# Optimization experiments

Measured on AMD Instinct MI355X. Metric: run time of the kernel, lower is better.

The kernel has to match this reference:

```python
import jax, jax.numpy as jnp
import numpy as np

K = 3
UP_H, UP_W = 120, 160  # up_size
RES_H, RES_W = UP_H + K - 1, UP_W + K - 1  # bilinear target before valid depthwise conv


def _bilinear_align_corners(x, out_h, out_w):
    """PyTorch UpsamplingBilinear2d (align_corners=True). x: [B,C,H,W]."""
    B, C, H, W = x.shape
    # row interpolation
    hy = jnp.arange(out_h, dtype=x.dtype) * ((H - 1) / (out_h - 1))
    y0 = jnp.floor(hy).astype(jnp.int32)
    y1 = jnp.minimum(y0 + 1, H - 1)
    fy = (hy - y0.astype(x.dtype))[None, None, :, None]
    x = x[:, :, y0, :] * (1 - fy) + x[:, :, y1, :] * fy  # [B,C,out_h,W]
    # col interpolation
    wx = jnp.arange(out_w, dtype=x.dtype) * ((W - 1) / (out_w - 1))
    x0i = jnp.floor(wx).astype(jnp.int32)
    x1i = jnp.minimum(x0i + 1, W - 1)
    fx = (wx - x0i.astype(x.dtype))[None, None, None, :]
    return x[:, :, :, x0i] * (1 - fx) + x[:, :, :, x1i] * fx  # [B,C,out_h,out_w]


def setup_inputs() -> dict:
    key = jax.random.key(0)
    k1, k2, k3 = jax.random.split(key, 3)
    C_in, C_out = 256, 128
    x = jax.random.normal(k1, (8, C_in, 60, 80), dtype=jnp.float32)
    # depthwise kernel [C_in, 1, K, K], pointwise [C_out, C_in]; fan-in-ish scale
    w_dw = jax.random.normal(k2, (C_in, 1, K, K), dtype=jnp.float32) * (1.0 / K)
    w_pw = jax.random.normal(k3, (C_out, C_in), dtype=jnp.float32) * (1.0 / np.sqrt(C_in))
    return {"x": x, "w_dw": w_dw, "w_pw": w_pw}


def reference(x, w_dw, w_pw):
    C_in = x.shape[1]
    # 1) bilinear upsample (align_corners=True) to (UP_H+K-1, UP_W+K-1)
    up = _bilinear_align_corners(x, RES_H, RES_W)
    # 2) depthwise KxK conv, stride 1, VALID padding -> [B,C_in,UP_H,UP_W]
    dw = jax.lax.conv_general_dilated(
        up, w_dw, window_strides=(1, 1), padding="VALID",
        dimension_numbers=("NCHW", "OIHW", "NCHW"),
        feature_group_count=C_in)
    # 3) pointwise 1x1 conv -> [B,C_out,UP_H,UP_W]
    return jnp.einsum("bchw,oc->bohw", dw, w_pw)
```

## Files before the change

kernel.cpp:

```cpp
#include <hip/hip_runtime.h>

#define CIN  256
#define HIN  60
#define WIN  80
#define UPH  120
#define UPW  160
#define COUT 128
#define NPIX (UPH*UPW)

typedef __bf16 bf16x8 __attribute__((ext_vector_type(8)));
typedef float  floatx4 __attribute__((ext_vector_type(4)));

__global__ void wpw_cvt(const float* __restrict__ wpw, __bf16* __restrict__ wpwb)
{
    int i = (blockIdx.x * blockDim.x + threadIdx.x) * 8;
    float4 a = *(const float4*)(wpw + i);
    float4 b = *(const float4*)(wpw + i + 4);
    bf16x8 o = {(__bf16)a.x,(__bf16)a.y,(__bf16)a.z,(__bf16)a.w,
                (__bf16)b.x,(__bf16)b.y,(__bf16)b.z,(__bf16)b.w};
    *(bf16x8*)(wpwb + i) = o;
}

#define F_NT  512
#define KC    32
#define NCK   (CIN/KC)
#define QPC   45
#define NIT   (KC*QPC)
#define NITP  1472

__global__ __launch_bounds__(F_NT, 4) void fused_kernel(
    const float* __restrict__ x,
    const float* __restrict__ wdw,
    const __bf16* __restrict__ wpwb,
    float* __restrict__ out)
{
    __shared__ __align__(16) float  s_xf[2][NITP*4];
    __shared__ __align__(16) __bf16 s_dw[2][160*KC];
    __shared__ float s_A[KC*19];
    __shared__ float s_rw[18];

    const int tid = threadIdx.x;

    const int bid = blockIdx.x;
    const int wg  = (bid & 7) * 120 + (bid >> 3);
    const int wt  = wg & 1;
    const int t2  = wg >> 1;
    const int ht  = t2 % 60;
    const int b   = t2 / 60;

    const int h0 = ht * 2, w0 = wt * 80;
    const float HS = 59.0f / 121.0f, WS = 79.0f / 161.0f;
    const int rbase = (int)((float)h0 * HS);
    const int c0a = ((int)((float)w0 * WS)) & ~3;

    if (tid < 18) {
        int ahh = tid / 9, t = tid - ahh * 9;
        int i3 = t / 3, dy = t - i3 * 3;
        int ybh = (int)((float)(h0 + ahh) * HS);
        float hy = (float)(h0 + ahh + i3) * HS;
        int y0 = (int)hy; float fy = hy - (float)y0;
        int y1 = min(y0 + 1, HIN - 1);
        s_rw[tid] = ((y0 - ybh) == dy ? 1.f - fy : 0.f)
                  + ((y1 - ybh) == dy ? fy : 0.f);
    }

    const int lane = tid & 63, wave = tid >> 6;
    const int quad = lane >> 4, l16 = lane & 15;

    const int ch  = tid & 31;
    const int seg = (tid >> 5) & 7;
    const int hh  = tid >> 8;
    const int rbh = (int)((float)(h0 + hh) * HS) - rbase;

    const int ciA = tid / 18, tA = tid - ciA * 18;
    const int hhA = tA / 9, dA = tA - hhA * 9, dyA = dA / 3, jA = dA - dyA * 3;
    const bool hasB = (tid < 64);
    const int iB = tid + 512, ciB = iB / 18, tB = iB - ciB * 18;
    const int hhB = tB / 9, dB = tB - hhB * 9, dyB = dB / 3, jB = dB - dyB * 3;

    const float* xb = x + (size_t)b * CIN * (HIN * WIN);

    auto dma = [&](int cb, int buf) {
        #pragma unroll
        for (int k = 0; k < 3; k++) {
            int ws = (k * 8 + wave) * 64;
            if (ws < NIT) {
                int it = ws + lane;
                it = it < NIT ? it : NIT - 1;
                int c  = it / QPC;
                int t  = it - c * QPC;
                t = t < 44 ? t : 43;
                int r = t / 11, q = t - r * 11;
                int gy = min(rbase + r, HIN - 1);
                const float* src = xb + (size_t)(cb + c) * (HIN * WIN)
                                 + gy * WIN + c0a + q * 4;
                __builtin_amdgcn_global_load_lds(
                    (const __attribute__((address_space(1))) void*)src,
                    (__attribute__((address_space(3))) void*)(&s_xf[buf][ws * 4]),
                    16, 0, 0);
            }
        }
    };

    float wA0, wA1, wA2, wB0 = 0.f, wB1 = 0.f, wB2 = 0.f;
    auto loadw = [&](int cb) {
        const float* wp = wdw + (size_t)(cb + ciA) * 9 + jA;
        wA0 = wp[0]; wA1 = wp[3]; wA2 = wp[6];
        if (hasB) {
            const float* wq = wdw + (size_t)(cb + ciB) * 9 + jB;
            wB0 = wq[0]; wB1 = wq[3]; wB2 = wq[6];
        }
    };

    floatx4 acc[10];
    #pragma unroll
    for (int n = 0; n < 10; n++) acc[n] = (floatx4){0.f, 0.f, 0.f, 0.f};

    dma(0, 0);
    loadw(0);
    __syncthreads();

    for (int p = 0; p < NCK; p++) {
        s_A[ciA * 19 + tA] = s_rw[hhA*9 + dyA]     * wA0
                           + s_rw[hhA*9 + 3 + dyA] * wA1
                           + s_rw[hhA*9 + 6 + dyA] * wA2;
        if (hasB)
            s_A[ciB * 19 + tB] = s_rw[hhB*9 + dyB]     * wB0
                               + s_rw[hhB*9 + 3 + dyB] * wB1
                               + s_rw[hhB*9 + 6 + dyB] * wB2;

        asm volatile("s_waitcnt vmcnt(0)" ::: "memory");
        __syncthreads();

        if (p < NCK - 1) {
            dma((p + 1) * KC, (p + 1) & 1);
            loadw((p + 1) * KC);
        }

        float Ar[3][3];
        #pragma unroll
        for (int dy = 0; dy < 3; dy++)
            #pragma unroll
            for (int j = 0; j < 3; j++)
                Ar[dy][j] = s_A[ch * 19 + hh * 9 + dy * 3 + j];

        const float* xfp = s_xf[p & 1];
        const int chb = ch * 180;
        __bf16* dwp = s_dw[p & 1];

        #pragma unroll
        for (int g = 0; g < 2; g++) {
            const int ub = w0 + seg * 10 + g * 5;
            float fx[7]; int ci[7];
            #pragma unroll
            for (int j = 0; j < 7; j++) {
                float wx = (float)(ub + j) * WS;
                int x0 = (int)wx;
                fx[j] = wx - (float)x0;
                ci[j] = chb + (x0 - c0a);
            }
            float d[5] = {0.f, 0.f, 0.f, 0.f, 0.f};
            #pragma unroll
            for (int dy = 0; dy < 3; dy++) {
                const float* rp = xfp + (rbh + dy) * 44;
                float cx[7];
                #pragma unroll
                for (int j = 0; j < 7; j++) {
                    float lo = rp[ci[j]], hi = rp[ci[j] + 1];
                    cx[j] = fmaf(fx[j], hi - lo, lo);
                }
                float A0 = Ar[dy][0], A1 = Ar[dy][1], A2 = Ar[dy][2];
                #pragma unroll
                for (int i = 0; i < 5; i++)
                    d[i] = fmaf(A0, cx[i],
                           fmaf(A1, cx[i+1],
                           fmaf(A2, cx[i+2], d[i])));
            }
            #pragma unroll
            for (int i = 0; i < 5; i++) {
                int px = hh * 80 + seg * 10 + g * 5 + i;
                dwp[px * KC + (ch ^ ((px & 3) << 3))] = (__bf16)d[i];
            }
        }

        bf16x8 af = *(const bf16x8*)(wpwb + (size_t)(wave * 16 + l16) * CIN
                                     + p * KC + quad * 8);

        __syncthreads();

        const char* dwb = (const char*)dwp;
        const int dwrd_base = l16 * 64 + ((quad * 16) ^ ((l16 & 3) << 4));
        #pragma unroll
        for (int n = 0; n < 10; n++) {
            bf16x8 bf = *(const bf16x8*)(dwb + dwrd_base + n * 1024);
            acc[n] = __builtin_amdgcn_mfma_f32_16x16x32_bf16(af, bf, acc[n], 0, 0, 0);
        }
    }

    float* ob = out + (size_t)(b * COUT + wave * 16 + quad * 4) * NPIX
              + (size_t)h0 * UPW + w0;
    #pragma unroll
    for (int n = 0; n < 10; n++) {
        int rowl = (n >= 5) ? 1 : 0;
        int col  = n * 16 + l16 - rowl * 80;
        float* pp = ob + (size_t)rowl * UPW + col;
        #pragma unroll
        for (int e = 0; e < 4; e++)
            __builtin_nontemporal_store(acc[n][e], pp + (size_t)e * NPIX);
    }
}

extern "C" void kernel_launch(void* const* d_in, const int* in_sizes, int n_in,
                              void* d_out, int out_size, void* d_ws, size_t ws_size,
                              hipStream_t stream)
{
    const float* x   = (const float*)d_in[0];
    const float* wdw = (const float*)d_in[1];
    const float* wpw = (const float*)d_in[2];

    wpw_cvt<<<dim3((COUT*CIN)/(256*8)), 256, 0, stream>>>(wpw, (__bf16*)d_ws);
    fused_kernel<<<dim3(960), F_NT, 0, stream>>>(
        x, wdw, (const __bf16*)d_ws, (float*)d_out);
}
```

Before: 247.0 us.

## Restructure fused kernel with triple-buffered 16-channel phases and in-kernel weight conversion

Drops the separate weight-conversion launch: pointwise weights are converted to bf16 into registers at kernel start, and all depthwise-times-row-weight coefficients are precomputed once into shared memory. The channel loop becomes 16-channel phases with a three-deep async global-to-LDS buffer and explicit waitcnt and barrier fencing. MFMA runs every other phase on 32 channels. The output is staged through LDS so it can be written with 16-byte coalesced stores. The aim is less launch overhead, fewer barriers and stalls, and better store coalescing, at the cost of higher LDS use and more register pressure from holding eight weight fragments.

```diff
diff --git a/kernel.cpp b/kernel.cpp
--- a/kernel.cpp
+++ b/kernel.cpp
@@ -11,33 +11,31 @@
 typedef __bf16 bf16x8 __attribute__((ext_vector_type(8)));
 typedef float  floatx4 __attribute__((ext_vector_type(4)));
 
-__global__ void wpw_cvt(const float* __restrict__ wpw, __bf16* __restrict__ wpwb)
-{
-    int i = (blockIdx.x * blockDim.x + threadIdx.x) * 8;
-    float4 a = *(const float4*)(wpw + i);
-    float4 b = *(const float4*)(wpw + i + 4);
-    bf16x8 o = {(__bf16)a.x,(__bf16)a.y,(__bf16)a.z,(__bf16)a.w,
-                (__bf16)b.x,(__bf16)b.y,(__bf16)b.z,(__bf16)b.w};
-    *(bf16x8*)(wpwb + i) = o;
-}
-
 #define F_NT  512
-#define KC    32
-#define NCK   (CIN/KC)
-#define QPC   45
-#define NIT   (KC*QPC)
-#define NITP  1472
+#define NPH   16
+#define GPC   48
+#define NG    768
+#define XFB   12288
+
+#define OFF_XF    0
+#define OFF_DW    36864
+#define OFF_A     49664
+#define OFF_RW    68096
+#define OFF_SCRAP 68176
+#define SMEM_SZ   69200
+
+#define FENCE __builtin_amdgcn_sched_barrier(0)
 
 __global__ __launch_bounds__(F_NT, 4) void fused_kernel(
     const float* __restrict__ x,
     const float* __restrict__ wdw,
-    const __bf16* __restrict__ wpwb,
+    const float* __restrict__ wpw,
     float* __restrict__ out)
 {
-    __shared__ __align__(16) float  s_xf[2][NITP*4];
-    __shared__ __align__(16) __bf16 s_dw[2][160*KC];
-    __shared__ float s_A[KC*19];
-    __shared__ float s_rw[18];
+    __shared__ __align__(16) char smem[SMEM_SZ];
+    float*  s_rw = (float*)(smem + OFF_RW);
+    float*  s_A  = (float*)(smem + OFF_A);
+    __bf16* s_dw = (__bf16*)(smem + OFF_DW);
 
     const int tid = threadIdx.x;
 
@@ -51,7 +49,7 @@
     const int h0 = ht * 2, w0 = wt * 80;
     const float HS = 59.0f / 121.0f, WS = 79.0f / 161.0f;
     const int rbase = (int)((float)h0 * HS);
-    const int c0a = ((int)((float)w0 * WS)) & ~3;
+    const int c0a   = ((int)((float)w0 * WS)) & ~3;
 
     if (tid < 18) {
         int ahh = tid / 9, t = tid - ahh * 9;
@@ -67,146 +65,161 @@
     const int lane = tid & 63, wave = tid >> 6;
     const int quad = lane >> 4, l16 = lane & 15;
 
-    const int ch  = tid & 31;
-    const int seg = (tid >> 5) & 7;
-    const int hh  = tid >> 8;
+    const int chl = tid >> 5;
+    const int g   = (tid >> 4) & 1;
+    const int hh  = (tid >> 3) & 1;
+    const int s   = tid & 7;
     const int rbh = (int)((float)(h0 + hh) * HS) - rbase;
 
-    const int ciA = tid / 18, tA = tid - ciA * 18;
-    const int hhA = tA / 9, dA = tA - hhA * 9, dyA = dA / 3, jA = dA - dyA * 3;
-    const bool hasB = (tid < 64);
-    const int iB = tid + 512, ciB = iB / 18, tB = iB - ciB * 18;
-    const int hhB = tB / 9, dB = tB - hhB * 9, dyB = dB / 3, jB = dB - dyB * 3;
-
     const float* xb = x + (size_t)b * CIN * (HIN * WIN);
 
-    auto dma = [&](int cb, int buf) {
-        #pragma unroll
-        for (int k = 0; k < 3; k++) {
-            int ws = (k * 8 + wave) * 64;
-            if (ws < NIT) {
-                int it = ws + lane;
-                it = it < NIT ? it : NIT - 1;
-                int c  = it / QPC;
-                int t  = it - c * QPC;
-                t = t < 44 ? t : 43;
-                int r = t / 11, q = t - r * 11;
-                int gy = min(rbase + r, HIN - 1);
-                const float* src = xb + (size_t)(cb + c) * (HIN * WIN)
-                                 + gy * WIN + c0a + q * 4;
-                __builtin_amdgcn_global_load_lds(
-                    (const __attribute__((address_space(1))) void*)src,
-                    (__attribute__((address_space(3))) void*)(&s_xf[buf][ws * 4]),
-                    16, 0, 0);
+    bf16x8 af[8];
+    #pragma unroll
+    for (int c = 0; c < 8; ++c) {
+        const float* wr = wpw + (size_t)(wave * 16 + l16) * CIN + c * 32 + quad * 8;
+        float4 v0 = *(const float4*)wr;
+        float4 v1 = *(const float4*)(wr + 4);
+        af[c] = (bf16x8){(__bf16)v0.x,(__bf16)v0.y,(__bf16)v0.z,(__bf16)v0.w,
+                         (__bf16)v1.x,(__bf16)v1.y,(__bf16)v1.z,(__bf16)v1.w};
+    }
+
+    __syncthreads();
+
+    #pragma unroll
+    for (int k = 0; k < 9; ++k) {
+        int i = tid + k * F_NT;
+        int gch = i / 18, t = i - gch * 18;
+        int h2 = t / 9, t9 = t - h2 * 9, dy = t9 / 3, j = t9 - dy * 3;
+        const float* wp = wdw + gch * 9 + j;
+        s_A[gch * 18 + t] = s_rw[h2*9 + dy]     * wp[0]
+                          + s_rw[h2*9 + 3 + dy] * wp[3]
+                          + s_rw[h2*9 + 6 + dy] * wp[6];
+    }
+
+    auto dma = [&](int cb, char* dst) {
+        {
+            int it = wave * 64 + lane;
+            int c = it / GPC, t = it - c * GPC;
+            int r = t / 12, q = t - r * 12; q = min(q, 10);
+            const float* src = xb + (size_t)(cb + c) * (HIN * WIN)
+                             + min(rbase + r, HIN - 1) * WIN + c0a + q * 4;
+            __builtin_amdgcn_global_load_lds(
+                (const __attribute__((address_space(1))) void*)src,
+                (__attribute__((address_space(3))) void*)(dst + (size_t)(wave * 64) * 16),
+                16, 0, 0);
+        }
+        {
+            int it = 512 + (wave & 3) * 64 + lane;
+            int c = it / GPC, t = it - c * GPC;
+            int r = t / 12, q = t - r * 12; q = min(q, 10);
+            const float* src = xb + (size_t)(cb + c) * (HIN * WIN)
+                             + min(rbase + r, HIN - 1) * WIN + c0a + q * 4;
+            char* d = (wave < 4) ? (dst + (size_t)(512 + (wave & 3) * 64) * 16)
+                                 : (smem + OFF_SCRAP);
+            __builtin_amdgcn_global_load_lds(
+                (const __attribute__((address_space(1))) void*)src,
+                (__attribute__((address_space(3))) void*)d,
+                16, 0, 0);
+        }
+    };
+
+    floatx4 acc[10];
+    #pragma unroll
+    for (int n = 0; n < 10; ++n) acc[n] = (floatx4){0.f, 0.f, 0.f, 0.f};
+
+    dma(0, smem + OFF_XF);
+    dma(16, smem + OFF_XF + XFB);
+
+    #pragma unroll
+    for (int h = 0; h < NPH; ++h) {
+        if (h < NPH - 1) asm volatile("s_waitcnt lgkmcnt(0) vmcnt(2)" ::: "memory");
+        else             asm volatile("s_waitcnt lgkmcnt(0) vmcnt(0)" ::: "memory");
+        FENCE; __builtin_amdgcn_s_barrier(); FENCE;
+
+        if (h + 2 < NPH) dma((h + 2) * 16, smem + OFF_XF + ((h + 2) % 3) * XFB);
+
+        const float* xf = (const float*)(smem + OFF_XF + (h % 3) * XFB);
+        const float* Ab = s_A + (h * 16 + chl) * 18 + hh * 9;
+        float Ar[3][3];
+        #pragma unroll
+        for (int dy = 0; dy < 3; ++dy)
+            #pragma unroll
+            for (int j = 0; j < 3; ++j) Ar[dy][j] = Ab[dy * 3 + j];
+
+        const int ub = w0 + s * 10 + g * 5;
+        float fx[7]; int ci[7];
+        #pragma unroll
+        for (int j = 0; j < 7; ++j) {
+            float wx = (float)(ub + j) * WS;
+            int x0 = (int)wx;
+            fx[j] = wx - (float)x0;
+            ci[j] = x0 - c0a;
+        }
+        float d[5] = {0.f, 0.f, 0.f, 0.f, 0.f};
+        #pragma unroll
+        for (int dy = 0; dy < 3; ++dy) {
+            const float* rp = xf + chl * 192 + (rbh + dy) * 48;
+            float cx[7];
+            #pragma unroll
+            for (int j = 0; j < 7; ++j) {
+                float lo = rp[ci[j]], hi = rp[ci[j] + 1];
+                cx[j] = fmaf(fx[j], hi - lo, lo);
             }
-        }
-    };
-
-    float wA0, wA1, wA2, wB0 = 0.f, wB1 = 0.f, wB2 = 0.f;
-    auto loadw = [&](int cb) {
-        const float* wp = wdw + (size_t)(cb + ciA) * 9 + jA;
-        wA0 = wp[0]; wA1 = wp[3]; wA2 = wp[6];
-        if (hasB) {
-            const float* wq = wdw + (size_t)(cb + ciB) * 9 + jB;
-            wB0 = wq[0]; wB1 = wq[3]; wB2 = wq[6];
-        }
-    };
-
-    floatx4 acc[10];
-    #pragma unroll
-    for (int n = 0; n < 10; n++) acc[n] = (floatx4){0.f, 0.f, 0.f, 0.f};
-
-    dma(0, 0);
-    loadw(0);
-    __syncthreads();
-
-    for (int p = 0; p < NCK; p++) {
-        s_A[ciA * 19 + tA] = s_rw[hhA*9 + dyA]     * wA0
-                           + s_rw[hhA*9 + 3 + dyA] * wA1
-                           + s_rw[hhA*9 + 6 + dyA] * wA2;
-        if (hasB)
-            s_A[ciB * 19 + tB] = s_rw[hhB*9 + dyB]     * wB0
-                               + s_rw[hhB*9 + 3 + dyB] * wB1
-                               + s_rw[hhB*9 + 6 + dyB] * wB2;
-
-        asm volatile("s_waitcnt vmcnt(0)" ::: "memory");
-        __syncthreads();
-
-        if (p < NCK - 1) {
-            dma((p + 1) * KC, (p + 1) & 1);
-            loadw((p + 1) * KC);
-        }
-
-        float Ar[3][3];
-        #pragma unroll
-        for (int dy = 0; dy < 3; dy++)
-            #pragma unroll
-            for (int j = 0; j < 3; j++)
-                Ar[dy][j] = s_A[ch * 19 + hh * 9 + dy * 3 + j];
-
-        const float* xfp = s_xf[p & 1];
-        const int chb = ch * 180;
-        __bf16* dwp = s_dw[p & 1];
-
-        #pragma unroll
-        for (int g = 0; g < 2; g++) {
-            const int ub = w0 + seg * 10 + g * 5;
-            float fx[7]; int ci[7];
-            #pragma unroll
-            for (int j = 0; j < 7; j++) {
-                float wx = (float)(ub + j) * WS;
-                int x0 = (int)wx;
-                fx[j] = wx - (float)x0;
-                ci[j] = chb + (x0 - c0a);
+            float A0 = Ar[dy][0], A1 = Ar[dy][1], A2 = Ar[dy][2];
+            #pragma unroll
+            for (int i = 0; i < 5; ++i)
+                d[i] = fmaf(A0, cx[i], fmaf(A1, cx[i+1], fmaf(A2, cx[i+2], d[i])));
+        }
+        {
+            const int kk = (h & 1) * 16 + chl;
+            const int kg = kk >> 3, kl = kk & 7;
+            #pragma unroll
+            for (int i = 0; i < 5; ++i) {
+                int px = hh * 80 + s * 10 + g * 5 + i;
+                s_dw[px * 40 + ((kg ^ (px & 3)) << 3) + kl] = (__bf16)d[i];
             }
-            float d[5] = {0.f, 0.f, 0.f, 0.f, 0.f};
-            #pragma unroll
-            for (int dy = 0; dy < 3; dy++) {
-                const float* rp = xfp + (rbh + dy) * 44;
-                float cx[7];
-                #pragma unroll
-                for (int j = 0; j < 7; j++) {
-                    float lo = rp[ci[j]], hi = rp[ci[j] + 1];
-                    cx[j] = fmaf(fx[j], hi - lo, lo);
-                }
-                float A0 = Ar[dy][0], A1 = Ar[dy][1], A2 = Ar[dy][2];
-                #pragma unroll
-                for (int i = 0; i < 5; i++)
-                    d[i] = fmaf(A0, cx[i],
-                           fmaf(A1, cx[i+1],
-                           fmaf(A2, cx[i+2], d[i])));
+        }
+
+        if (h & 1) {
+            asm volatile("s_waitcnt lgkmcnt(0)" ::: "memory");
+            FENCE; __builtin_amdgcn_s_barrier(); FENCE;
+            const int c = h >> 1;
+            #pragma unroll
+            for (int n = 0; n < 10; ++n) {
+                const __bf16* bp = s_dw + (n * 16 + l16) * 40
+                                 + ((quad ^ (l16 & 3)) << 3);
+                bf16x8 bf = *(const bf16x8*)bp;
+                acc[n] = __builtin_amdgcn_mfma_f32_16x16x32_bf16(af[c], bf, acc[n], 0, 0, 0);
             }
-            #pragma unroll
-            for (int i = 0; i < 5; i++) {
-                int px = hh * 80 + seg * 10 + g * 5 + i;
-                dwp[px * KC + (ch ^ ((px & 3) << 3))] = (__bf16)d[i];
-            }
-        }
-
-        bf16x8 af = *(const bf16x8*)(wpwb + (size_t)(wave * 16 + l16) * CIN
-                                     + p * KC + quad * 8);
-
-        __syncthreads();
-
-        const char* dwb = (const char*)dwp;
-        const int dwrd_base = l16 * 64 + ((quad * 16) ^ ((l16 & 3) << 4));
-        #pragma unroll
-        for (int n = 0; n < 10; n++) {
-            bf16x8 bf = *(const bf16x8*)(dwb + dwrd_base + n * 1024);
-            acc[n] = __builtin_amdgcn_mfma_f32_16x16x32_bf16(af, bf, acc[n], 0, 0, 0);
-        }
-    }
-
-    float* ob = out + (size_t)(b * COUT + wave * 16 + quad * 4) * NPIX
-              + (size_t)h0 * UPW + w0;
-    #pragma unroll
-    for (int n = 0; n < 10; n++) {
-        int rowl = (n >= 5) ? 1 : 0;
-        int col  = n * 16 + l16 - rowl * 80;
-        float* pp = ob + (size_t)rowl * UPW + col;
-        #pragma unroll
-        for (int e = 0; e < 4; e++)
-            __builtin_nontemporal_store(acc[n][e], pp + (size_t)e * NPIX);
+        }
+    }
+
+    asm volatile("s_waitcnt lgkmcnt(0)" ::: "memory");
+    FENCE; __builtin_amdgcn_s_barrier(); FENCE;
+
+    float* tb = (float*)smem;
+    const int rr = tid >> 2, sg = tid & 3;
+    #pragma unroll
+    for (int rowl = 0; rowl < 2; ++rowl) {
+        #pragma unroll
+        for (int n = 0; n < 5; ++n)
+            #pragma unroll
+            for (int e = 0; e < 4; ++e)
+                tb[(wave * 16 + quad * 4 + e) * 84 + n * 16 + l16] = acc[rowl * 5 + n][e];
+
+        asm volatile("s_waitcnt lgkmcnt(0)" ::: "memory");
+        FENCE; __builtin_amdgcn_s_barrier(); FENCE;
+
+        float* op = out + (size_t)(b * COUT + rr) * NPIX
+                  + (size_t)(h0 + rowl) * UPW + w0 + sg * 20;
+        #pragma unroll
+        for (int i = 0; i < 5; ++i) {
+            floatx4 v = *(const floatx4*)&tb[rr * 84 + sg * 20 + i * 4];
+            __builtin_nontemporal_store(v, (floatx4*)(op + i * 4));
+        }
+
+        asm volatile("s_waitcnt lgkmcnt(0)" ::: "memory");
+        FENCE; __builtin_amdgcn_s_barrier(); FENCE;
     }
 }
 
@@ -214,11 +227,10 @@
                               void* d_out, int out_size, void* d_ws, size_t ws_size,
                               hipStream_t stream)
 {
+    (void)d_ws; (void)ws_size;
     const float* x   = (const float*)d_in[0];
     const float* wdw = (const float*)d_in[1];
     const float* wpw = (const float*)d_in[2];
 
-    wpw_cvt<<<dim3((COUT*CIN)/(256*8)), 256, 0, stream>>>(wpw, (__bf16*)d_ws);
-    fused_kernel<<<dim3(960), F_NT, 0, stream>>>(
-        x, wdw, (const __bf16*)d_ws, (float*)d_out);
+    fused_kernel<<<dim3(960), F_NT, 0, stream>>>(x, wdw, wpw, (float*)d_out);
 }
```

Result: slower. 310.4 us (+25.7%).
